# Kernel optimization log

Hardware: AMD Instinct MI355X
Metric: run time of the kernel (lower is better)

The kernel has to match this reference:

```python
import math
import jax, jax.numpy as jnp
import numpy as np

NUM_BUCKETS = 32
MAX_DISTANCE = 128
N_HEADS = 16
D_KV = 64


def _relative_position_bucket(rel_pos, num_buckets=NUM_BUCKETS, max_distance=MAX_DISTANCE):
    # bidirectional=True branch of T5's bucketing
    num_buckets = num_buckets // 2
    rel_buckets = (rel_pos > 0).astype(jnp.int32) * num_buckets
    rel_pos = jnp.abs(rel_pos)
    max_exact = num_buckets // 2
    is_small = rel_pos < max_exact
    # safe log (values < max_exact are masked out by is_small)
    rp_f = jnp.maximum(rel_pos, 1).astype(jnp.float32)
    rel_if_large = max_exact + (
        jnp.log(rp_f / max_exact) / math.log(max_distance / max_exact) * (num_buckets - max_exact)
    ).astype(jnp.int32)
    rel_if_large = jnp.minimum(rel_if_large, num_buckets - 1)
    return rel_buckets + jnp.where(is_small, rel_pos, rel_if_large)


def compute_bias(rel_bias_table, q_len, k_len):
    ctx = jnp.arange(q_len)[:, None]
    mem = jnp.arange(k_len)[None, :]
    buckets = _relative_position_bucket(mem - ctx)  # [q, k]
    values = rel_bias_table[buckets]                # [q, k, h]
    return jnp.transpose(values, (2, 0, 1))[None]   # [1, h, q, k]


def setup_inputs() -> dict:
    key = jax.random.key(0)
    k1, k2, k3, k4 = jax.random.split(key, 4)
    d_model = 1024
    return {
        "hidden_states": jax.random.normal(k1, (2, 2048, d_model), jnp.float32),
        "w_qkv": jax.random.normal(k2, (d_model, 3 * N_HEADS * D_KV), jnp.float32) * (d_model ** -0.5),
        "w_o": jax.random.normal(k3, (N_HEADS * D_KV, d_model), jnp.float32) * ((N_HEADS * D_KV) ** -0.5),
        "rel_bias_table": jax.random.normal(k4, (NUM_BUCKETS, N_HEADS), jnp.float32),
    }


def reference(hidden_states, w_qkv, w_o, rel_bias_table):
    b, s, _ = hidden_states.shape
    inner = N_HEADS * D_KV
    qkv = hidden_states @ w_qkv                         # [b, s, 3*inner]
    q, k, v = jnp.split(qkv, [inner, 2 * inner], axis=-1)
    def to_bhsd(x):
        return jnp.transpose(x.reshape(b, s, N_HEADS, D_KV), (0, 2, 1, 3))
    q, k, v = to_bhsd(q), to_bhsd(k), to_bhsd(v)
    scores = jnp.einsum("bhqd,bhkd->bhqk", q, k)        # no 1/sqrt(d) scaling in T5
    position_bias = compute_bias(rel_bias_table, s, s)  # [1, h, q, k]
    scores = scores + position_bias
    attn = jax.nn.softmax(scores.astype(jnp.float32), axis=-1).astype(scores.dtype)
    out = jnp.einsum("bhqk,bhkd->bhqd", attn, v)
    out = jnp.transpose(out, (0, 2, 1, 3)).reshape(b, s, inner)
    attn_output = out @ w_o
    return attn_output, position_bias
```

## Files before the change

### kernel.cpp

```cpp
#include <hip/hip_runtime.h>
#include <hip/hip_bf16.h>
#include <cstdint>
#include <cstddef>

#define S_LEN 2048
#define NH 16
#define DKV 64
#define BATCH 2
#define DMODEL 1024

typedef _Float16 half_t;
typedef __attribute__((ext_vector_type(4))) _Float16 halfx4;
typedef __attribute__((ext_vector_type(8))) _Float16 half8;
typedef __attribute__((ext_vector_type(4))) float floatx4;

__device__ __forceinline__ void load_lds16(const half_t* g, half_t* l) {
  __builtin_amdgcn_global_load_lds((const __attribute__((address_space(1))) void*)g,
                                   (__attribute__((address_space(3))) void*)l, 16, 0, 0);
}

__device__ __forceinline__ int t5_bucket(int delta) {
  int base = (delta > 0) ? 16 : 0;
  int a = delta < 0 ? -delta : delta;
  int n;
  if (a < 8)       n = a;
  else if (a < 12) n = 8;
  else if (a < 16) n = 9;
  else if (a < 23) n = 10;
  else if (a < 32) n = 11;
  else if (a < 46) n = 12;
  else if (a < 64) n = 13;
  else if (a < 91) n = 14;
  else             n = 15;
  return base + n;
}

__global__ __launch_bounds__(256) void bias_kernel(const float* __restrict__ table,
                                                   float* __restrict__ out) {
  int h = blockIdx.x >> 11;
  int q = blockIdx.x & (S_LEN - 1);
  __shared__ float tb[32];
  if (threadIdx.x < 32) tb[threadIdx.x] = table[threadIdx.x * NH + h];
  __syncthreads();
  float* dst = out + (size_t)blockIdx.x * S_LEN;
  int k0 = threadIdx.x * 4;
#pragma unroll
  for (int half = 0; half < 2; half++) {
    int k = k0 + half * 1024;
    float4 v;
    v.x = tb[t5_bucket((k + 0) - q)];
    v.y = tb[t5_bucket((k + 1) - q)];
    v.z = tb[t5_bucket((k + 2) - q)];
    v.w = tb[t5_bucket((k + 3) - q)];
    *(float4*)(dst + k) = v;
  }
}

__global__ __launch_bounds__(256) void cast_f2h(const float* __restrict__ in,
                                                half_t* __restrict__ out) {
  int i = blockIdx.x * 256 + threadIdx.x;
  float4 v = ((const float4*)in)[i];
  halfx4 h;
  h[0] = (half_t)v.x; h[1] = (half_t)v.y; h[2] = (half_t)v.z; h[3] = (half_t)v.w;
  ((halfx4*)out)[i] = h;
}

__global__ __launch_bounds__(256) void transpose_cast(const float* __restrict__ in,
                                                      half_t* __restrict__ out,
                                                      int R, int C) {
  __shared__ float t[32][33];
  int lr = threadIdx.x >> 3;
  int lc = (threadIdx.x & 7) * 4;
  int r0 = blockIdx.y * 32, c0 = blockIdx.x * 32;
  float4 v = *(const float4*)(in + (size_t)(r0 + lr) * C + c0 + lc);
  t[lr][lc + 0] = v.x; t[lr][lc + 1] = v.y; t[lr][lc + 2] = v.z; t[lr][lc + 3] = v.w;
  __syncthreads();
  halfx4 hv;
#pragma unroll
  for (int u = 0; u < 4; u++) hv[u] = (half_t)t[lc + u][lr];
  *(halfx4*)(out + (size_t)(c0 + lr) * R + r0 + lc) = hv;
}

__global__ __launch_bounds__(256) void vtrans(const half_t* __restrict__ V,
                                              half_t* __restrict__ Vt) {
  __shared__ half_t T[64 * 72];
  const int bh = blockIdx.y;
  const int s0 = blockIdx.x * 64;
  const half_t* src = V + ((size_t)bh * S_LEN + s0) * DKV;
  half_t* dst = Vt + (size_t)bh * DKV * S_LEN + s0;
  const int sr = threadIdx.x >> 3;
  const int dc = (threadIdx.x & 7) * 8;
#pragma unroll
  for (int p = 0; p < 2; p++) {
    int s = sr + p * 32;
    half8 v = *(const half8*)(src + (size_t)s * DKV + dc);
#pragma unroll
    for (int u = 0; u < 8; u++) T[(dc + u) * 72 + s] = v[u];
  }
  __syncthreads();
#pragma unroll
  for (int p = 0; p < 2; p++) {
    int d = sr + p * 32;
    half8 v = *(half8*)&T[d * 72 + dc];
    *(half8*)(dst + (size_t)d * S_LEN + dc) = v;
  }
}

template <int MODE>
__global__ __launch_bounds__(256) void hgemm128(const half_t* __restrict__ A,
                                                const half_t* __restrict__ Bt,
                                                float* __restrict__ C,
                                                half_t* __restrict__ Qo,
                                                half_t* __restrict__ Ko,
                                                half_t* __restrict__ Vo,
                                                int M, int N, int K) {
  __shared__ half_t Asl[8 * 512];
  __shared__ half_t Bsl[8 * 512];

  const int tid = threadIdx.x;
  const int w = tid >> 6;
  const int lane = tid & 63;
  const int l15 = lane & 15;
  const int quad = lane >> 4;
  const int wm = w >> 1, wn = w & 1;
  const int m0 = blockIdx.y * 128;
  const int n0 = blockIdx.x * 128;

  floatx4 acc[4][4];
#pragma unroll
  for (int i = 0; i < 4; i++)
#pragma unroll
    for (int j = 0; j < 4; j++) acc[i][j] = (floatx4){0.f, 0.f, 0.f, 0.f};

  const half_t* ga0 = A + (size_t)(m0 + (2 * w + 0) * 16 + l15) * K + quad * 8;
  const half_t* ga1 = A + (size_t)(m0 + (2 * w + 1) * 16 + l15) * K + quad * 8;
  const half_t* gb0 = Bt + (size_t)(n0 + (2 * w + 0) * 16 + l15) * K + quad * 8;
  const half_t* gb1 = Bt + (size_t)(n0 + (2 * w + 1) * 16 + l15) * K + quad * 8;
  half_t* la0 = &Asl[(2 * w + 0) * 512];
  half_t* la1 = &Asl[(2 * w + 1) * 512];
  half_t* lb0 = &Bsl[(2 * w + 0) * 512];
  half_t* lb1 = &Bsl[(2 * w + 1) * 512];

  for (int k0 = 0; k0 < K; k0 += 32) {
    __syncthreads();
    load_lds16(ga0 + k0, la0);
    load_lds16(ga1 + k0, la1);
    load_lds16(gb0 + k0, lb0);
    load_lds16(gb1 + k0, lb1);
    __syncthreads();

    half8 af[4], bf[4];
#pragma unroll
    for (int i = 0; i < 4; i++) af[i] = *(half8*)&Asl[(wm * 4 + i) * 512 + lane * 8];
#pragma unroll
    for (int j = 0; j < 4; j++) bf[j] = *(half8*)&Bsl[(wn * 4 + j) * 512 + lane * 8];
#pragma unroll
    for (int i = 0; i < 4; i++)
#pragma unroll
      for (int j = 0; j < 4; j++)
        acc[i][j] = __builtin_amdgcn_mfma_f32_16x16x32_f16(af[i], bf[j], acc[i][j], 0, 0, 0);
  }

  const int rowbase = m0 + wm * 64;
  const int colbase = n0 + wn * 64;
  if (MODE == 0) {
#pragma unroll
    for (int i = 0; i < 4; i++)
#pragma unroll
      for (int j = 0; j < 4; j++)
#pragma unroll
        for (int r = 0; r < 4; r++)
          C[(size_t)(rowbase + i * 16 + quad * 4 + r) * N + colbase + j * 16 + l15] =
              acc[i][j][r];
  } else {
    const int which = colbase >> 10;
    const int h = (colbase & 1023) >> 6;
    const int b = rowbase >> 11;
    const int s0 = rowbase & (S_LEN - 1);
    half_t* base = ((which == 0) ? Qo : (which == 1) ? Ko : Vo) +
                   (size_t)(b * NH + h) * S_LEN * DKV;
#pragma unroll
    for (int i = 0; i < 4; i++)
#pragma unroll
      for (int j = 0; j < 4; j++)
#pragma unroll
        for (int r = 0; r < 4; r++)
          base[(size_t)(s0 + i * 16 + quad * 4 + r) * DKV + j * 16 + l15] =
              (half_t)acc[i][j][r];
  }
}

__global__ __launch_bounds__(256) void attn_split(const half_t* __restrict__ Q,
                                                  const half_t* __restrict__ K,
                                                  const half_t* __restrict__ Vt,
                                                  const float* __restrict__ table,
                                                  float* __restrict__ Opart,
                                                  float* __restrict__ Mp,
                                                  float* __restrict__ Lp) {
  __shared__ half_t Ks[64 * 64];
  __shared__ half_t Vts[64 * 64];
  __shared__ half_t Ps[64 * 68];
  __shared__ float tb[32];
  __shared__ float ebias[184];

  const int tid = threadIdx.x;
  const int w = tid >> 6;
  const int lane = tid & 63;
  const int l15 = lane & 15;
  const int quad = lane >> 4;
  const int bh = blockIdx.y;
  const int h = bh & (NH - 1);
  const int part = blockIdx.x & 1;
  const int q0 = (blockIdx.x >> 1) * 64;
  const int q0w = q0 + w * 16;

  if (tid < 32) tb[tid] = table[tid * NH + h];
  __syncthreads();
  if (tid < 183) ebias[tid] = __expf(tb[t5_bucket(tid - 91)]);

  half8 qf[2];
#pragma unroll
  for (int ks = 0; ks < 2; ks++)
    qf[ks] = *(const half8*)(Q + ((size_t)bh * S_LEN + q0w + l15) * DKV +
                             ks * 32 + quad * 8);

  floatx4 o[4];
  float m[4], l[4];
#pragma unroll
  for (int r = 0; r < 4; r++) { m[r] = -1e30f; l[r] = 0.0f; }
#pragma unroll
  for (int nb = 0; nb < 4; nb++) o[nb] = (floatx4){0.f, 0.f, 0.f, 0.f};

  const int jr = tid >> 2;
  const int ub = (tid & 3) * 2;
  const int kbase = part * 1024;

  for (int kc = kbase; kc < kbase + 1024; kc += 64) {
    __syncthreads();
    {
      const half_t* Kg = K + ((size_t)bh * S_LEN + kc + jr) * DKV + ub * 8;
      const half_t* Vg = Vt + ((size_t)bh * DKV + jr) * S_LEN + kc + ub * 8;
      half8 k0v = *(const half8*)(Kg);
      half8 k1v = *(const half8*)(Kg + 8);
      half8 v0v = *(const half8*)(Vg);
      half8 v1v = *(const half8*)(Vg + 8);
      int sw = jr & 7;
      *(half8*)&Ks[jr * 64 + ((ub + 0) ^ sw) * 8] = k0v;
      *(half8*)&Ks[jr * 64 + ((ub + 1) ^ sw) * 8] = k1v;
      *(half8*)&Vts[jr * 64 + ((ub + 0) ^ sw) * 8] = v0v;
      *(half8*)&Vts[jr * 64 + ((ub + 1) ^ sw) * 8] = v1v;
    }
    __syncthreads();

    floatx4 s[4];
#pragma unroll
    for (int nb = 0; nb < 4; nb++) {
      s[nb] = (floatx4){0.f, 0.f, 0.f, 0.f};
      int key = nb * 16 + l15;
      int sw = key & 7;
#pragma unroll
      for (int ks = 0; ks < 2; ks++) {
        half8 bf = *(half8*)&Ks[key * 64 + ((ks * 4 + quad) ^ sw) * 8];
        s[nb] = __builtin_amdgcn_mfma_f32_16x16x32_f16(qf[ks], bf, s[nb], 0, 0, 0);
      }
    }

    const int rel = kc - q0w;
    float al[4];
    if (rel >= 106 || rel <= -154) {
      const float eb = ebias[rel >= 106 ? 182 : 0];
#pragma unroll
      for (int r = 0; r < 4; r++) {
        float cm = fmaxf(fmaxf(s[0][r], s[1][r]), fmaxf(s[2][r], s[3][r]));
#pragma unroll
        for (int msk = 1; msk <= 8; msk <<= 1) cm = fmaxf(cm, __shfl_xor(cm, msk));
        float mn = fmaxf(m[r], cm);
        al[r] = __expf(m[r] - mn);
        m[r] = mn;
        float psum = 0.0f;
#pragma unroll
        for (int nb = 0; nb < 4; nb++) {
          float p = __expf(s[nb][r] - mn) * eb;
          psum += p;
          Ps[(w * 16 + quad * 4 + r) * 68 + nb * 16 + l15] = (half_t)p;
        }
#pragma unroll
        for (int msk = 1; msk <= 8; msk <<= 1) psum += __shfl_xor(psum, msk);
        l[r] = l[r] * al[r] + psum;
#pragma unroll
        for (int nb = 0; nb < 4; nb++) o[nb][r] *= al[r];
      }
    } else {
#pragma unroll
      for (int r = 0; r < 4; r++) {
        int qabs = q0w + quad * 4 + r;
        int db = kc + l15 - qabs + 91;
        float cm = fmaxf(fmaxf(s[0][r], s[1][r]), fmaxf(s[2][r], s[3][r]));
#pragma unroll
        for (int msk = 1; msk <= 8; msk <<= 1) cm = fmaxf(cm, __shfl_xor(cm, msk));
        float mn = fmaxf(m[r], cm);
        al[r] = __expf(m[r] - mn);
        m[r] = mn;
        float psum = 0.0f;
#pragma unroll
        for (int nb = 0; nb < 4; nb++) {
          int idx = db + nb * 16;
          idx = idx < 0 ? 0 : (idx > 182 ? 182 : idx);
          float p = __expf(s[nb][r] - mn) * ebias[idx];
          psum += p;
          Ps[(w * 16 + quad * 4 + r) * 68 + nb * 16 + l15] = (half_t)p;
        }
#pragma unroll
        for (int msk = 1; msk <= 8; msk <<= 1) psum += __shfl_xor(psum, msk);
        l[r] = l[r] * al[r] + psum;
#pragma unroll
        for (int nb = 0; nb < 4; nb++) o[nb][r] *= al[r];
      }
    }

    half8 af[2];
#pragma unroll
    for (int ks = 0; ks < 2; ks++)
      af[ks] = *(half8*)&Ps[(w * 16 + l15) * 68 + ks * 32 + quad * 8];
#pragma unroll
    for (int nb = 0; nb < 4; nb++) {
      int dd = nb * 16 + l15;
      int sw = dd & 7;
#pragma unroll
      for (int ks = 0; ks < 2; ks++) {
        half8 bf = *(half8*)&Vts[dd * 64 + ((ks * 4 + quad) ^ sw) * 8];
        o[nb] = __builtin_amdgcn_mfma_f32_16x16x32_f16(af[ks], bf, o[nb], 0, 0, 0);
      }
    }
  }

#pragma unroll
  for (int r = 0; r < 4; r++) {
    int row = bh * S_LEN + q0w + quad * 4 + r;
    float* op = Opart + (size_t)part * 4194304 + (size_t)row * 64;
#pragma unroll
    for (int nb = 0; nb < 4; nb++) op[nb * 16 + l15] = o[nb][r];
    if (l15 == 0) {
      Mp[part * 65536 + row] = m[r];
      Lp[part * 65536 + row] = l[r];
    }
  }
}

__global__ __launch_bounds__(256) void attn_combine(const float* __restrict__ Opart,
                                                    const float* __restrict__ Mp,
                                                    const float* __restrict__ Lp,
                                                    half_t* __restrict__ X) {
  int idx = blockIdx.x * 256 + threadIdx.x;
  int row = idx >> 6;
  int d = idx & 63;
  float m0 = Mp[row], m1 = Mp[65536 + row];
  float l0 = Lp[row], l1 = Lp[65536 + row];
  float M = fmaxf(m0, m1);
  float a0 = __expf(m0 - M), a1 = __expf(m1 - M);
  float L = l0 * a0 + l1 * a1;
  float o = (Opart[(size_t)row * 64 + d] * a0 +
             Opart[4194304 + (size_t)row * 64 + d] * a1) / L;
  int bh = row >> 11, q = row & (S_LEN - 1);
  int b = bh >> 4, h = bh & (NH - 1);
  X[(size_t)(b * S_LEN + q) * DMODEL + h * DKV + d] = (half_t)o;
}

extern "C" void kernel_launch(void* const* d_in, const int* in_sizes, int n_in,
                              void* d_out, int out_size, void* d_ws, size_t ws_size,
                              hipStream_t stream) {
  const float* hidden = (const float*)d_in[0];
  const float* w_qkv = (const float*)d_in[1];
  const float* w_o = (const float*)d_in[2];
  const float* table = (const float*)d_in[3];

  float* attn_out = (float*)d_out;
  float* bias_out = (float*)d_out + 4194304;

  half_t* Ah  = (half_t*)d_ws;
  half_t* Wqt = Ah + 4194304;
  half_t* Wot = Wqt + 3145728;
  half_t* Qh  = Wot + 1048576;
  half_t* Kh  = Qh + 4194304;
  half_t* Vh  = Kh + 4194304;
  half_t* Xh  = Vh + 4194304;
  half_t* Vth = Ah;
  float* Opart = (float*)(Xh + 4194304);
  float* Mpp   = Opart + 8388608;
  float* Lpp   = Mpp + 131072;

  cast_f2h<<<4096, 256, 0, stream>>>(hidden, Ah);
  transpose_cast<<<dim3(3072 / 32, 1024 / 32), 256, 0, stream>>>(w_qkv, Wqt, 1024, 3072);
  transpose_cast<<<dim3(1024 / 32, 1024 / 32), 256, 0, stream>>>(w_o, Wot, 1024, 1024);
  bias_kernel<<<NH * S_LEN, 256, 0, stream>>>(table, bias_out);

  hgemm128<1><<<dim3(3072 / 128, 4096 / 128), 256, 0, stream>>>(
      Ah, Wqt, nullptr, Qh, Kh, Vh, 4096, 3072, 1024);

  vtrans<<<dim3(S_LEN / 64, BATCH * NH), 256, 0, stream>>>(Vh, Vth);

  attn_split<<<dim3((S_LEN / 64) * 2, BATCH * NH), 256, 0, stream>>>(
      Qh, Kh, Vth, table, Opart, Mpp, Lpp);
  attn_combine<<<4194304 / 256, 256, 0, stream>>>(Opart, Mpp, Lpp, Xh);

  hgemm128<0><<<dim3(1024 / 128, 4096 / 128), 256, 0, stream>>>(
      Xh, Wot, attn_out, nullptr, nullptr, nullptr, 4096, 1024, 1024);
}
```

Measured before the change: 525.3 us.

## Compute row sums via MFMA, add bias in exponent, deepen GEMM k-step

The attention kernel now adds the relative bias inside the exponent rather than multiplying by a precomputed exp(bias). Row sums of P come from an extra MFMA against a ones vector, which replaces the shuffle reductions. Max reductions use ds_swizzle, and address arithmetic is hoisted out of the loop. The QKV/output GEMM doubles its K step per barrier pair to 64 with larger LDS tiles, and launch bounds add occupancy hints. The row sum is now taken from the fp16-rounded P values, which changes numerics slightly, and the larger LDS footprint may reduce GEMM occupancy.

```diff
diff --git a/kernel.cpp b/kernel.cpp
--- a/kernel.cpp
+++ b/kernel.cpp
@@ -17,6 +17,15 @@
 __device__ __forceinline__ void load_lds16(const half_t* g, half_t* l) {
   __builtin_amdgcn_global_load_lds((const __attribute__((address_space(1))) void*)g,
                                    (__attribute__((address_space(3))) void*)l, 16, 0, 0);
+}
+
+__device__ __forceinline__ float qmax16(float v) {
+  int i;
+  i = __builtin_amdgcn_ds_swizzle(__float_as_int(v), 0x041F); v = fmaxf(v, __int_as_float(i));
+  i = __builtin_amdgcn_ds_swizzle(__float_as_int(v), 0x081F); v = fmaxf(v, __int_as_float(i));
+  i = __builtin_amdgcn_ds_swizzle(__float_as_int(v), 0x101F); v = fmaxf(v, __int_as_float(i));
+  i = __builtin_amdgcn_ds_swizzle(__float_as_int(v), 0x201F); v = fmaxf(v, __int_as_float(i));
+  return v;
 }
 
 __device__ __forceinline__ int t5_bucket(int delta) {
@@ -107,15 +116,15 @@
 }
 
 template <int MODE>
-__global__ __launch_bounds__(256) void hgemm128(const half_t* __restrict__ A,
-                                                const half_t* __restrict__ Bt,
-                                                float* __restrict__ C,
-                                                half_t* __restrict__ Qo,
-                                                half_t* __restrict__ Ko,
-                                                half_t* __restrict__ Vo,
-                                                int M, int N, int K) {
-  __shared__ half_t Asl[8 * 512];
-  __shared__ half_t Bsl[8 * 512];
+__global__ __launch_bounds__(256, 4) void hgemm128(const half_t* __restrict__ A,
+                                                   const half_t* __restrict__ Bt,
+                                                   float* __restrict__ C,
+                                                   half_t* __restrict__ Qo,
+                                                   half_t* __restrict__ Ko,
+                                                   half_t* __restrict__ Vo,
+                                                   int M, int N, int K) {
+  __shared__ half_t Asl[16 * 512];
+  __shared__ half_t Bsl[16 * 512];
 
   const int tid = threadIdx.x;
   const int w = tid >> 6;
@@ -132,33 +141,48 @@
 #pragma unroll
     for (int j = 0; j < 4; j++) acc[i][j] = (floatx4){0.f, 0.f, 0.f, 0.f};
 
-  const half_t* ga0 = A + (size_t)(m0 + (2 * w + 0) * 16 + l15) * K + quad * 8;
-  const half_t* ga1 = A + (size_t)(m0 + (2 * w + 1) * 16 + l15) * K + quad * 8;
-  const half_t* gb0 = Bt + (size_t)(n0 + (2 * w + 0) * 16 + l15) * K + quad * 8;
-  const half_t* gb1 = Bt + (size_t)(n0 + (2 * w + 1) * 16 + l15) * K + quad * 8;
-  half_t* la0 = &Asl[(2 * w + 0) * 512];
-  half_t* la1 = &Asl[(2 * w + 1) * 512];
-  half_t* lb0 = &Bsl[(2 * w + 0) * 512];
-  half_t* lb1 = &Bsl[(2 * w + 1) * 512];
-
-  for (int k0 = 0; k0 < K; k0 += 32) {
+  const half_t* ga[2][2];
+  const half_t* gb[2][2];
+  half_t* la[2][2];
+  half_t* lb[2][2];
+#pragma unroll
+  for (int b = 0; b < 2; b++)
+#pragma unroll
+    for (int ks = 0; ks < 2; ks++) {
+      ga[b][ks] = A + (size_t)(m0 + (2 * w + b) * 16 + l15) * K + ks * 32 + quad * 8;
+      gb[b][ks] = Bt + (size_t)(n0 + (2 * w + b) * 16 + l15) * K + ks * 32 + quad * 8;
+      la[b][ks] = &Asl[((2 * w + b) * 2 + ks) * 512];
+      lb[b][ks] = &Bsl[((2 * w + b) * 2 + ks) * 512];
+    }
+
+  for (int k0 = 0; k0 < K; k0 += 64) {
     __syncthreads();
-    load_lds16(ga0 + k0, la0);
-    load_lds16(ga1 + k0, la1);
-    load_lds16(gb0 + k0, lb0);
-    load_lds16(gb1 + k0, lb1);
+#pragma unroll
+    for (int b = 0; b < 2; b++)
+#pragma unroll
+      for (int ks = 0; ks < 2; ks++) {
+        load_lds16(ga[b][ks], la[b][ks]);
+        load_lds16(gb[b][ks], lb[b][ks]);
+        ga[b][ks] += 64;
+        gb[b][ks] += 64;
+      }
     __syncthreads();
 
-    half8 af[4], bf[4];
-#pragma unroll
-    for (int i = 0; i < 4; i++) af[i] = *(half8*)&Asl[(wm * 4 + i) * 512 + lane * 8];
-#pragma unroll
-    for (int j = 0; j < 4; j++) bf[j] = *(half8*)&Bsl[(wn * 4 + j) * 512 + lane * 8];
-#pragma unroll
-    for (int i = 0; i < 4; i++)
+#pragma unroll
+    for (int ks = 0; ks < 2; ks++) {
+      half8 af[4], bf[4];
+#pragma unroll
+      for (int i = 0; i < 4; i++)
+        af[i] = *(half8*)&Asl[((wm * 4 + i) * 2 + ks) * 512 + lane * 8];
 #pragma unroll
       for (int j = 0; j < 4; j++)
-        acc[i][j] = __builtin_amdgcn_mfma_f32_16x16x32_f16(af[i], bf[j], acc[i][j], 0, 0, 0);
+        bf[j] = *(half8*)&Bsl[((wn * 4 + j) * 2 + ks) * 512 + lane * 8];
+#pragma unroll
+      for (int i = 0; i < 4; i++)
+#pragma unroll
+        for (int j = 0; j < 4; j++)
+          acc[i][j] = __builtin_amdgcn_mfma_f32_16x16x32_f16(af[i], bf[j], acc[i][j], 0, 0, 0);
+    }
   }
 
   const int rowbase = m0 + wm * 64;
@@ -190,18 +214,18 @@
   }
 }
 
-__global__ __launch_bounds__(256) void attn_split(const half_t* __restrict__ Q,
-                                                  const half_t* __restrict__ K,
-                                                  const half_t* __restrict__ Vt,
-                                                  const float* __restrict__ table,
-                                                  float* __restrict__ Opart,
-                                                  float* __restrict__ Mp,
-                                                  float* __restrict__ Lp) {
+__global__ __launch_bounds__(256, 6) void attn_split(const half_t* __restrict__ Q,
+                                                     const half_t* __restrict__ K,
+                                                     const half_t* __restrict__ Vt,
+                                                     const float* __restrict__ table,
+                                                     float* __restrict__ Opart,
+                                                     float* __restrict__ Mp,
+                                                     float* __restrict__ Lp) {
   __shared__ half_t Ks[64 * 64];
   __shared__ half_t Vts[64 * 64];
   __shared__ half_t Ps[64 * 68];
   __shared__ float tb[32];
-  __shared__ float ebias[184];
+  __shared__ float badd[184];
 
   const int tid = threadIdx.x;
   const int w = tid >> 6;
@@ -211,12 +235,12 @@
   const int bh = blockIdx.y;
   const int h = bh & (NH - 1);
   const int part = blockIdx.x & 1;
-  const int q0 = (blockIdx.x >> 1) * 64;
-  const int q0w = q0 + w * 16;
+  const int q0w = (blockIdx.x >> 1) * 64 + w * 16;
 
   if (tid < 32) tb[tid] = table[tid * NH + h];
   __syncthreads();
-  if (tid < 183) ebias[tid] = __expf(tb[t5_bucket(tid - 91)]);
+  if (tid < 183) badd[tid] = tb[t5_bucket(tid - 91)];
+  const float tb_neg = tb[15], tb_pos = tb[31];
 
   half8 qf[2];
 #pragma unroll
@@ -224,27 +248,37 @@
     qf[ks] = *(const half8*)(Q + ((size_t)bh * S_LEN + q0w + l15) * DKV +
                              ks * 32 + quad * 8);
 
-  floatx4 o[4];
-  float m[4], l[4];
-#pragma unroll
-  for (int r = 0; r < 4; r++) { m[r] = -1e30f; l[r] = 0.0f; }
+  half8 bones;
+#pragma unroll
+  for (int j = 0; j < 8; j++) bones[j] = (l15 == 0) ? (half_t)1.0f : (half_t)0.0f;
+
+  floatx4 o[4], oL;
+  float m[4];
+#pragma unroll
+  for (int r = 0; r < 4; r++) m[r] = -1e30f;
 #pragma unroll
   for (int nb = 0; nb < 4; nb++) o[nb] = (floatx4){0.f, 0.f, 0.f, 0.f};
+  oL = (floatx4){0.f, 0.f, 0.f, 0.f};
 
   const int jr = tid >> 2;
   const int ub = (tid & 3) * 2;
-  const int kbase = part * 1024;
-
-  for (int kc = kbase; kc < kbase + 1024; kc += 64) {
+  const int sw = jr & 7;
+  const int kv_rd0 = l15 * 64 + ((0 * 4 + quad) ^ (l15 & 7)) * 8;
+  const int kv_rd1 = l15 * 64 + ((1 * 4 + quad) ^ (l15 & 7)) * 8;
+  const int ps_wr = (w * 16 + quad * 4) * 68 + l15;
+  const int ps_rd = (w * 16 + l15) * 68 + quad * 8;
+
+  const half_t* Kg = K + ((size_t)bh * S_LEN + part * 1024 + jr) * DKV + ub * 8;
+  const half_t* Vg = Vt + ((size_t)bh * DKV + jr) * S_LEN + part * 1024 + ub * 8;
+  int rel = part * 1024 - q0w;
+
+  for (int it = 0; it < 16; it++, rel += 64, Kg += 64 * DKV, Vg += 64) {
     __syncthreads();
     {
-      const half_t* Kg = K + ((size_t)bh * S_LEN + kc + jr) * DKV + ub * 8;
-      const half_t* Vg = Vt + ((size_t)bh * DKV + jr) * S_LEN + kc + ub * 8;
       half8 k0v = *(const half8*)(Kg);
       half8 k1v = *(const half8*)(Kg + 8);
       half8 v0v = *(const half8*)(Vg);
       half8 v1v = *(const half8*)(Vg + 8);
-      int sw = jr & 7;
       *(half8*)&Ks[jr * 64 + ((ub + 0) ^ sw) * 8] = k0v;
       *(half8*)&Ks[jr * 64 + ((ub + 1) ^ sw) * 8] = k1v;
       *(half8*)&Vts[jr * 64 + ((ub + 0) ^ sw) * 8] = v0v;
@@ -256,82 +290,64 @@
 #pragma unroll
     for (int nb = 0; nb < 4; nb++) {
       s[nb] = (floatx4){0.f, 0.f, 0.f, 0.f};
-      int key = nb * 16 + l15;
-      int sw = key & 7;
-#pragma unroll
-      for (int ks = 0; ks < 2; ks++) {
-        half8 bf = *(half8*)&Ks[key * 64 + ((ks * 4 + quad) ^ sw) * 8];
-        s[nb] = __builtin_amdgcn_mfma_f32_16x16x32_f16(qf[ks], bf, s[nb], 0, 0, 0);
-      }
-    }
-
-    const int rel = kc - q0w;
+      s[nb] = __builtin_amdgcn_mfma_f32_16x16x32_f16(
+          qf[0], *(half8*)&Ks[nb * 1024 + kv_rd0], s[nb], 0, 0, 0);
+      s[nb] = __builtin_amdgcn_mfma_f32_16x16x32_f16(
+          qf[1], *(half8*)&Ks[nb * 1024 + kv_rd1], s[nb], 0, 0, 0);
+    }
+
     float al[4];
     if (rel >= 106 || rel <= -154) {
-      const float eb = ebias[rel >= 106 ? 182 : 0];
+      const float lb = (rel >= 106) ? tb_pos : tb_neg;
 #pragma unroll
       for (int r = 0; r < 4; r++) {
-        float cm = fmaxf(fmaxf(s[0][r], s[1][r]), fmaxf(s[2][r], s[3][r]));
-#pragma unroll
-        for (int msk = 1; msk <= 8; msk <<= 1) cm = fmaxf(cm, __shfl_xor(cm, msk));
+        float cm = qmax16(fmaxf(fmaxf(s[0][r], s[1][r]), fmaxf(s[2][r], s[3][r])));
         float mn = fmaxf(m[r], cm);
         al[r] = __expf(m[r] - mn);
         m[r] = mn;
-        float psum = 0.0f;
-#pragma unroll
-        for (int nb = 0; nb < 4; nb++) {
-          float p = __expf(s[nb][r] - mn) * eb;
-          psum += p;
-          Ps[(w * 16 + quad * 4 + r) * 68 + nb * 16 + l15] = (half_t)p;
-        }
-#pragma unroll
-        for (int msk = 1; msk <= 8; msk <<= 1) psum += __shfl_xor(psum, msk);
-        l[r] = l[r] * al[r] + psum;
+        float sh = lb - mn;
+#pragma unroll
+        for (int nb = 0; nb < 4; nb++)
+          Ps[ps_wr + r * 68 + nb * 16] = (half_t)__expf(s[nb][r] + sh);
 #pragma unroll
         for (int nb = 0; nb < 4; nb++) o[nb][r] *= al[r];
+        oL[r] *= al[r];
       }
     } else {
 #pragma unroll
       for (int r = 0; r < 4; r++) {
-        int qabs = q0w + quad * 4 + r;
-        int db = kc + l15 - qabs + 91;
-        float cm = fmaxf(fmaxf(s[0][r], s[1][r]), fmaxf(s[2][r], s[3][r]));
-#pragma unroll
-        for (int msk = 1; msk <= 8; msk <<= 1) cm = fmaxf(cm, __shfl_xor(cm, msk));
+        int db = rel + l15 - (quad * 4 + r) + 91;
+        float bv[4];
+#pragma unroll
+        for (int nb = 0; nb < 4; nb++) {
+          int idx = db + nb * 16;
+          idx = idx < 0 ? 0 : (idx > 182 ? 182 : idx);
+          bv[nb] = badd[idx];
+        }
+        float cm = qmax16(fmaxf(fmaxf(s[0][r], s[1][r]), fmaxf(s[2][r], s[3][r])));
         float mn = fmaxf(m[r], cm);
         al[r] = __expf(m[r] - mn);
         m[r] = mn;
-        float psum = 0.0f;
-#pragma unroll
-        for (int nb = 0; nb < 4; nb++) {
-          int idx = db + nb * 16;
-          idx = idx < 0 ? 0 : (idx > 182 ? 182 : idx);
-          float p = __expf(s[nb][r] - mn) * ebias[idx];
-          psum += p;
-          Ps[(w * 16 + quad * 4 + r) * 68 + nb * 16 + l15] = (half_t)p;
-        }
-#pragma unroll
-        for (int msk = 1; msk <= 8; msk <<= 1) psum += __shfl_xor(psum, msk);
-        l[r] = l[r] * al[r] + psum;
+#pragma unroll
+        for (int nb = 0; nb < 4; nb++)
+          Ps[ps_wr + r * 68 + nb * 16] = (half_t)__expf(s[nb][r] - mn + bv[nb]);
 #pragma unroll
         for (int nb = 0; nb < 4; nb++) o[nb][r] *= al[r];
+        oL[r] *= al[r];
       }
     }
 
-    half8 af[2];
-#pragma unroll
-    for (int ks = 0; ks < 2; ks++)
-      af[ks] = *(half8*)&Ps[(w * 16 + l15) * 68 + ks * 32 + quad * 8];
+    half8 af0 = *(half8*)&Ps[ps_rd];
+    half8 af1 = *(half8*)&Ps[ps_rd + 32];
 #pragma unroll
     for (int nb = 0; nb < 4; nb++) {
-      int dd = nb * 16 + l15;
-      int sw = dd & 7;
-#pragma unroll
-      for (int ks = 0; ks < 2; ks++) {
-        half8 bf = *(half8*)&Vts[dd * 64 + ((ks * 4 + quad) ^ sw) * 8];
-        o[nb] = __builtin_amdgcn_mfma_f32_16x16x32_f16(af[ks], bf, o[nb], 0, 0, 0);
-      }
-    }
+      o[nb] = __builtin_amdgcn_mfma_f32_16x16x32_f16(
+          af0, *(half8*)&Vts[nb * 1024 + kv_rd0], o[nb], 0, 0, 0);
+      o[nb] = __builtin_amdgcn_mfma_f32_16x16x32_f16(
+          af1, *(half8*)&Vts[nb * 1024 + kv_rd1], o[nb], 0, 0, 0);
+    }
+    oL = __builtin_amdgcn_mfma_f32_16x16x32_f16(af0, bones, oL, 0, 0, 0);
+    oL = __builtin_amdgcn_mfma_f32_16x16x32_f16(af1, bones, oL, 0, 0, 0);
   }
 
 #pragma unroll
@@ -342,7 +358,7 @@
     for (int nb = 0; nb < 4; nb++) op[nb * 16 + l15] = o[nb][r];
     if (l15 == 0) {
       Mp[part * 65536 + row] = m[r];
-      Lp[part * 65536 + row] = l[r];
+      Lp[part * 65536 + row] = oL[r];
     }
   }
 }
```

New measurement: 542.8 us. +3.3%, slower.
